# Kernel tuning notes

Hardware: AMD Instinct MI355X
Metric: run time of the kernel (lower is better)

Reference implementation:

```python
import jax, jax.numpy as jnp
import numpy as np

DIM = 128; D_STATE = 16; D_CONV = 4; EXPAND = 2
D_INNER = DIM * EXPAND            # 256
DT_RANK = (DIM + 15) // 16        # 8
B, H, W = 2, 56, 56


def _ln(x, w, b):
    m = jnp.mean(x, -1, keepdims=True)
    v = jnp.var(x, -1, keepdims=True)
    return (x - m) * jax.lax.rsqrt(v + 1e-5) * w + b


def _mamba(x, in_w, conv_w, conv_b, xproj_w, dt_w, dt_b, A_log, Dp, out_w):
    # x: (B, L, DIM)
    Bb, L, _ = x.shape
    xz = x @ in_w.T                                   # (B,L,2*D_INNER)
    xi, z = jnp.split(xz, 2, axis=-1)
    # causal depthwise conv1d (pad left d_conv-1, truncate to L)
    xc = jnp.transpose(xi, (0, 2, 1))                 # (B,D_INNER,L)
    xc = jax.lax.conv_general_dilated(
        xc, conv_w, (1,), [(D_CONV - 1, 0)],
        dimension_numbers=('NCH', 'OIH', 'NCH'),
        feature_group_count=D_INNER) + conv_b[None, :, None]
    xs = jax.nn.silu(jnp.transpose(xc, (0, 2, 1)))    # (B,L,D_INNER)
    dbl = xs @ xproj_w.T                              # (B,L,DT_RANK+2*D_STATE)
    dt = jax.nn.softplus(dbl[..., :DT_RANK] @ dt_w.T + dt_b)   # (B,L,D_INNER)
    Bc = dbl[..., DT_RANK:DT_RANK + D_STATE]          # (B,L,D_STATE)
    Cc = dbl[..., DT_RANK + D_STATE:]                 # (B,L,D_STATE)
    A = -jnp.exp(A_log)                               # (D_INNER,D_STATE)
    dA = jnp.exp(dt[..., None] * A)                   # (B,L,D_INNER,D_STATE)
    dBu = (dt * xs)[..., None] * Bc[:, :, None, :]    # (B,L,D_INNER,D_STATE)

    def step(h, inp):
        a, bu, c = inp
        h = a * h + bu                                # (B,D_INNER,D_STATE)
        return h, jnp.einsum('bdn,bn->bd', h, c)

    h0 = jnp.zeros((Bb, D_INNER, D_STATE), x.dtype)
    _, ys = jax.lax.scan(step, h0, (jnp.moveaxis(dA, 1, 0),
                                    jnp.moveaxis(dBu, 1, 0),
                                    jnp.moveaxis(Cc, 1, 0)))
    y = jnp.moveaxis(ys, 0, 1) + xs * Dp              # (B,L,D_INNER)
    y = y * jax.nn.silu(z)
    return y @ out_w.T                                # (B,L,DIM)


def _forward(x, norm_h_w, norm_h_b, norm_v_w, norm_v_b,
             dw_w, dw_b, pw_w, pw_b,
             h_in_w, h_conv_w, h_conv_b, h_xproj_w, h_dt_w, h_dt_b, h_A_log, h_D, h_out_w,
             v_in_w, v_conv_w, v_conv_b, v_xproj_w, v_dt_w, v_dt_b, v_A_log, v_D, v_out_w,
             ca_fc1_w, ca_fc2_w):
    Bb, C, Hh, Ww = x.shape
    # local branch: depthwise 3x3 + GELU + 1x1
    lf = jax.lax.conv_general_dilated(
        x, dw_w, (1, 1), [(1, 1), (1, 1)],
        dimension_numbers=('NCHW', 'OIHW', 'NCHW'),
        feature_group_count=C) + dw_b[None, :, None, None]
    lf = jax.nn.gelu(lf, approximate=False)
    lf = jnp.einsum('bchw,oc->bohw', lf, pw_w[:, :, 0, 0]) + pw_b[None, :, None, None]
    # horizontal scan: row-major tokens
    xh = _ln(x.reshape(Bb, C, Hh * Ww).transpose(0, 2, 1), norm_h_w, norm_h_b)
    oh = _mamba(xh, h_in_w, h_conv_w, h_conv_b, h_xproj_w, h_dt_w, h_dt_b,
                h_A_log, h_D, h_out_w)
    oh = oh.transpose(0, 2, 1).reshape(Bb, C, Hh, Ww)
    # vertical scan: column-major tokens
    xv = _ln(jnp.transpose(x, (0, 1, 3, 2)).reshape(Bb, C, Ww * Hh).transpose(0, 2, 1),
             norm_v_w, norm_v_b)
    ov = _mamba(xv, v_in_w, v_conv_w, v_conv_b, v_xproj_w, v_dt_w, v_dt_b,
                v_A_log, v_D, v_out_w)
    ov = jnp.transpose(ov.transpose(0, 2, 1).reshape(Bb, C, Ww, Hh), (0, 1, 3, 2))
    fused = oh + ov + lf
    # channel attention
    y = jnp.mean(fused, axis=(2, 3))                  # (B,C)
    y = jax.nn.sigmoid(jax.nn.relu(y @ ca_fc1_w.T) @ ca_fc2_w.T)
    return fused * y[:, :, None, None] + x


def setup_inputs() -> dict:
    key = jax.random.key(0)
    ks = iter(jax.random.split(key, 64))
    def nrm(shape, scale):
        return jax.random.normal(next(ks), shape, jnp.float32) * scale
    d = {}
    d['x'] = nrm((B, DIM, H, W), 1.0)
    d['norm_h_w'] = jnp.ones((DIM,), jnp.float32); d['norm_h_b'] = jnp.zeros((DIM,), jnp.float32)
    d['norm_v_w'] = jnp.ones((DIM,), jnp.float32); d['norm_v_b'] = jnp.zeros((DIM,), jnp.float32)
    d['dw_w'] = nrm((DIM, 1, 3, 3), 1.0 / 3.0)
    d['dw_b'] = jnp.zeros((DIM,), jnp.float32)
    d['pw_w'] = nrm((DIM, DIM, 1, 1), DIM ** -0.5)
    d['pw_b'] = jnp.zeros((DIM,), jnp.float32)
    for p in ('h', 'v'):
        d[p + '_in_w'] = nrm((2 * D_INNER, DIM), DIM ** -0.5)
        d[p + '_conv_w'] = nrm((D_INNER, 1, D_CONV), D_CONV ** -0.5)
        d[p + '_conv_b'] = jnp.zeros((D_INNER,), jnp.float32)
        d[p + '_xproj_w'] = nrm((DT_RANK + 2 * D_STATE, D_INNER), D_INNER ** -0.5)
        d[p + '_dt_w'] = nrm((D_INNER, DT_RANK), DT_RANK ** -0.5)
        d[p + '_dt_b'] = jnp.full((D_INNER,), -2.0, jnp.float32)  # small positive dt
        d[p + '_A_log'] = jnp.log(jnp.tile(jnp.arange(1, D_STATE + 1, dtype=jnp.float32), (D_INNER, 1)))
        d[p + '_D'] = jnp.ones((D_INNER,), jnp.float32)
        d[p + '_out_w'] = nrm((DIM, D_INNER), D_INNER ** -0.5)
    d['ca_fc1_w'] = nrm((DIM // 4, DIM), DIM ** -0.5)
    d['ca_fc2_w'] = nrm((DIM, DIM // 4), (DIM // 4) ** -0.5)
    return d


def reference(x, norm_h_w, norm_h_b, norm_v_w, norm_v_b,
              dw_w, dw_b, pw_w, pw_b,
              h_in_w, h_conv_w, h_conv_b, h_xproj_w, h_dt_w, h_dt_b, h_A_log, h_D, h_out_w,
              v_in_w, v_conv_w, v_conv_b, v_xproj_w, v_dt_w, v_dt_b, v_A_log, v_D, v_out_w,
              ca_fc1_w, ca_fc2_w):
    return _forward(x, norm_h_w, norm_h_b, norm_v_w, norm_v_b,
                    dw_w, dw_b, pw_w, pw_b,
                    h_in_w, h_conv_w, h_conv_b, h_xproj_w, h_dt_w, h_dt_b, h_A_log, h_D, h_out_w,
                    v_in_w, v_conv_w, v_conv_b, v_xproj_w, v_dt_w, v_dt_b, v_A_log, v_D, v_out_w,
                    ca_fc1_w, ca_fc2_w)
```

## Files before the change

### kernel.cpp

```cpp
#include <hip/hip_runtime.h>
#include <hip/hip_bf16.h>

typedef __hip_bfloat16 bf16;
__device__ __forceinline__ float b2f(bf16 v){ return __bfloat162float(v); }
__device__ __forceinline__ bf16 f2b(float v){ return __float2bfloat16(v); }

typedef __attribute__((ext_vector_type(8))) short frag_ab;
typedef __attribute__((ext_vector_type(4))) float frag_cd;
typedef __attribute__((ext_vector_type(4))) short short4v;

__device__ __forceinline__ frag_ab ld_frag_2xb64(const bf16* p){
  union { frag_ab f; short4v h[2]; } u;
  u.h[0] = *reinterpret_cast<const short4v*>(p);
  u.h[1] = *reinterpret_cast<const short4v*>(p+4);
  return u.f;
}

#define LLEN 3136
#define BATCH 2
#define NCHUNK 49
#define LC 64

__global__ void k_front(const float* __restrict__ x, const float* __restrict__ dww,
                        const float* __restrict__ dwb, bf16* __restrict__ tmp,
                        const float* nhw_, const float* nhb_, const float* nvw_,
                        const float* nvb_, bf16* __restrict__ xln,
                        float* __restrict__ YMEAN){
  int blk = blockIdx.x;
  int tid = threadIdx.x;
  if (blk < 1024){
    int bc = blk & 255;
    int seg = blk >> 8;
    int c = bc & 127;
    if (bc == 0 && seg == 0 && tid < 256) YMEAN[tid] = 0.f;
    const float* xp = x + (size_t)bc*LLEN;
    float w[9];
    #pragma unroll
    for (int i=0;i<9;i++) w[i] = dww[c*9+i];
    float bias = dwb[c];
    int pstart = seg * 784;
    for (int p = pstart + tid; p < pstart + 784; p += 256){
      int i = p/56, j = p%56;
      float acc = bias;
      #pragma unroll
      for (int a=0;a<3;a++){
        int ii = i + a - 1;
        if (ii < 0 || ii >= 56) continue;
        #pragma unroll
        for (int bb=0;bb<3;bb++){
          int jj = j + bb - 1;
          if (jj < 0 || jj >= 56) continue;
          acc += w[a*3+bb] * xp[ii*56+jj];
        }
      }
      float g = 0.5f*acc*(1.0f + erff(acc*0.70710678118654752f));
      tmp[(size_t)bc*LLEN + p] = f2b(g);
    }
  } else {
    int idx2 = blk - 1024;
    int h = idx2 % 56, b = idx2 / 56;
    __shared__ float sx[128][57];
    __shared__ float smean[56], srstd[56];
    __shared__ float wh[128], bh[128], wv_[128], bv_[128];
    if (tid < 128){ wh[tid]=nhw_[tid]; bh[tid]=nhb_[tid];
                    wv_[tid]=nvw_[tid]; bv_[tid]=nvb_[tid]; }
    for (int idx = tid; idx < 128*56; idx += 256){
      int c = idx / 56, w = idx % 56;
      sx[c][w] = x[((size_t)(b*128+c))*LLEN + h*56 + w];
    }
    __syncthreads();
    if (tid < 56){
      float s=0.f, s2=0.f;
      for (int c=0;c<128;c++){ float v = sx[c][tid]; s+=v; s2+=v*v; }
      float m = s*(1.f/128.f);
      float var = s2*(1.f/128.f) - m*m;
      smean[tid]=m; srstd[tid]=rsqrtf(var+1e-5f);
    }
    __syncthreads();
    bf16* outh = xln;
    bf16* outv = xln + (size_t)BATCH*LLEN*128;
    for (int idx = tid; idx < 56*128; idx += 256){
      int w = idx >> 7, c = idx & 127;
      float v = (sx[c][w]-smean[w])*srstd[w];
      outh[((size_t)b*LLEN + h*56 + w)*128 + c] = f2b(v*wh[c]+bh[c]);
      outv[((size_t)b*LLEN + w*56 + h)*128 + c] = f2b(v*wv_[c]+bv_[c]);
    }
  }
}

__global__ void k_inproj(const bf16* __restrict__ xln, const float* __restrict__ hw,
                         const float* __restrict__ vw, bf16* __restrict__ XI, bf16* __restrict__ Z){
  int dir = blockIdx.z;
  const bf16* A = xln + (size_t)dir*BATCH*LLEN*128;
  const float* W = dir ? vw : hw;
  int m0 = blockIdx.x*64;
  int npair = blockIdx.y*128;
  __shared__ __align__(16) bf16 sA[64][136];
  __shared__ __align__(16) bf16 sW[64][136];
  int tid = threadIdx.x;
  #pragma unroll
  for (int r=0;r<4;r++){
    int idx = tid + r*256;
    int row = idx >> 4, c8 = (idx & 15)*8;
    *reinterpret_cast<float4*>(&sA[row][c8]) =
        *reinterpret_cast<const float4*>(&A[(size_t)(m0+row)*128 + c8]);
  }
  int wv2 = tid >> 6, lane = tid & 63;
  int qd = lane >> 4, mr = lane & 15;
  bf16* dst = (npair < 256) ? XI : Z;
  int nbase0 = npair & 255;
  size_t dslab = (size_t)dir*BATCH*LLEN*256;
  #pragma unroll
  for (int nt=0; nt<2; nt++){
    int n0 = npair + nt*64;
    __syncthreads();
    #pragma unroll
    for (int r=0;r<8;r++){
      int idx = tid + r*256;
      int row = idx >> 5, c4 = (idx & 31)*4;
      float4 w4 = *reinterpret_cast<const float4*>(&W[(size_t)(n0+row)*128 + c4]);
      bf16 t4[4] = {f2b(w4.x), f2b(w4.y), f2b(w4.z), f2b(w4.w)};
      *reinterpret_cast<double*>(&sW[row][c4]) = *reinterpret_cast<double*>(t4);
    }
    __syncthreads();
    frag_cd acc[4] = {};
    #pragma unroll
    for (int k0=0;k0<128;k0+=32){
      frag_ab af = *reinterpret_cast<frag_ab*>(&sA[wv2*16+mr][k0+qd*8]);
      #pragma unroll
      for (int t=0;t<4;t++){
        frag_ab bfr = *reinterpret_cast<frag_ab*>(&sW[t*16+mr][k0+qd*8]);
        acc[t] = __builtin_amdgcn_mfma_f32_16x16x32_bf16(af, bfr, acc[t], 0, 0, 0);
      }
    }
    int nb = nbase0 + nt*64;
    #pragma unroll
    for (int t=0;t<4;t++)
      #pragma unroll
      for (int r=0;r<4;r++){
        int row = m0 + wv2*16 + qd*4 + r;
        int col = nb + t*16 + mr;
        dst[dslab + (size_t)row*256 + col] = f2b(acc[t][r]);
      }
  }
}

__global__ void k_dbl(const bf16* __restrict__ XI,
                      const float* hcw, const float* hcb, const float* vcw, const float* vcb,
                      const float* __restrict__ hx, const float* __restrict__ vx,
                      const float* hdw, const float* vdw, const float* hdb, const float* vdb,
                      bf16* __restrict__ XS2, bf16* __restrict__ DT2,
                      float* __restrict__ Bf, float* __restrict__ Cf){
  int m0 = blockIdx.x*64;
  int bd = m0 / LLEN;
  int l0m = m0 % LLEN;
  int dirq = bd >> 1;
  const bf16* XId = XI + (size_t)bd*LLEN*256;
  const float* W = dirq ? vx : hx;
  const float* cw = dirq ? vcw : hcw;
  const float* cb = dirq ? vcb : hcb;
  __shared__ __align__(16) bf16 sA[67][264];
  __shared__ __align__(16) bf16 sW[48][264];
  __shared__ float sdbl[64][49];
  int tid = threadIdx.x;
  for (int idx = tid; idx < 67*32; idx += 256){
    int row = idx >> 5, c8 = (idx & 31)*8;
    int l = l0m - 3 + row;
    float4 v = make_float4(0.f,0.f,0.f,0.f);
    if (l >= 0) v = *reinterpret_cast<const float4*>(&XId[(size_t)l*256 + c8]);
    *reinterpret_cast<float4*>(&sA[row][c8]) = v;
  }
  #pragma unroll
  for (int r=0;r<12;r++){
    int idx = tid + r*256;
    int row = idx >> 6, c4 = (idx & 63)*4;
    bf16 t4[4] = {f2b(0.f), f2b(0.f), f2b(0.f), f2b(0.f)};
    if (row < 40){
      float4 w4 = *reinterpret_cast<const float4*>(&W[(size_t)row*256 + c4]);
      t4[0]=f2b(w4.x); t4[1]=f2b(w4.y); t4[2]=f2b(w4.z); t4[3]=f2b(w4.w);
    }
    *reinterpret_cast<double*>(&sW[row][c4]) = *reinterpret_cast<double*>(t4);
  }
  __syncthreads();
  {
    float w0=cw[tid*4], w1=cw[tid*4+1], w2=cw[tid*4+2], w3=cw[tid*4+3];
    float cbias = cb[tid];
    size_t x2base = ((size_t)bd*16 + (tid>>4))*LLEN + l0m;
    int c16 = tid & 15;
    float xm3 = b2f(sA[0][tid]), xm2 = b2f(sA[1][tid]), xm1 = b2f(sA[2][tid]);
    #pragma unroll 4
    for (int j=0;j<64;j++){
      float x0 = b2f(sA[j+3][tid]);
      float acc = cbias + w0*xm3 + w1*xm2 + w2*xm1 + w3*x0;
      float s = acc / (1.f + __expf(-acc));
      bf16 sv = f2b(s);
      sA[j][tid] = sv;
      XS2[(x2base + j)*16 + c16] = sv;
      xm3=xm2; xm2=xm1; xm1=x0;
    }
  }
  __syncthreads();
  int wv2 = tid >> 6, lane = tid & 63;
  int qd = lane >> 4, mr = lane & 15;
  frag_cd acc[3] = {};
  #pragma unroll
  for (int k0=0;k0<256;k0+=32){
    frag_ab af = *reinterpret_cast<frag_ab*>(&sA[wv2*16+mr][k0+qd*8]);
    #pragma unroll
    for (int t=0;t<3;t++){
      frag_ab bfr = *reinterpret_cast<frag_ab*>(&sW[t*16+mr][k0+qd*8]);
      acc[t] = __builtin_amdgcn_mfma_f32_16x16x32_bf16(af, bfr, acc[t], 0, 0, 0);
    }
  }
  #pragma unroll
  for (int t=0;t<3;t++)
    #pragma unroll
    for (int r=0;r<4;r++){
      int col = t*16 + mr;
      if (col < 40) sdbl[wv2*16 + qd*4 + r][col] = acc[t][r];
    }
  __syncthreads();
  const float* dtw = dirq ? vdw : hdw;
  const float* dtb = dirq ? vdb : hdb;
  float w8[8];
  #pragma unroll
  for (int r=0;r<8;r++) w8[r] = dtw[tid*8+r];
  float biasv = dtb[tid];
  size_t d2base = ((size_t)bd*16 + (tid>>4))*LLEN + l0m;
  int c16 = tid & 15;
  for (int row=0; row<64; row++){
    float a = biasv;
    #pragma unroll
    for (int r=0;r<8;r++) a += sdbl[row][r]*w8[r];
    float sv = (a > 20.f) ? a : __logf(1.f + __expf(a));
    DT2[(d2base + row)*16 + c16] = f2b(sv);
  }
  #pragma unroll
  for (int r=0;r<8;r++){
    int idx = tid + r*256;
    int row = idx >> 5, o = idx & 31;
    float v = sdbl[row][8+o];
    size_t rr = (size_t)(m0+row)*16;
    if (o < 16) Bf[rr + o] = v;
    else        Cf[rr + (o-16)] = v;
  }
}

__global__ void k_scan1(const bf16* __restrict__ DT2, const bf16* __restrict__ XS2,
                        const float* __restrict__ Bc, const float* hA, const float* vA,
                        float* __restrict__ Pbuf, float* __restrict__ Hbuf){
  int bd = blockIdx.z;
  int g  = blockIdx.y;
  int ck = blockIdx.x;
  int l0 = ck*LC;
  const float* Bd = Bc + (size_t)bd*LLEN*16;
  const float* Alog = (bd >> 1) ? vA : hA;
  int tid = threadIdx.x;
  int dl = tid >> 4, n = tid & 15;
  float A = -__expf(Alog[(g*16+dl)*16+n]);
  __shared__ float sdt[LC][16], sxs[LC][16], sB[LC][16];
  size_t base2 = (((size_t)bd*16 + g)*LLEN + l0)*16;
  #pragma unroll
  for (int r=0;r<4;r++){
    int idx = tid + r*256;
    sdt[idx>>4][idx&15] = b2f(DT2[base2 + idx]);
    sxs[idx>>4][idx&15] = b2f(XS2[base2 + idx]);
    (&sB[0][0])[idx] = Bd[(size_t)l0*16 + idx];
  }
  __syncthreads();
  float h = 0.f, P = 1.f;
  #pragma unroll 8
  for (int i=0;i<LC;i++){
    float a = sdt[i][dl];
    float u = sxs[i][dl];
    float dA = __expf(a * A);
    h = dA*h + (a*u)*sB[i][n];
    P *= dA;
  }
  size_t sidx = (((size_t)bd*16 + g)*NCHUNK + ck)*256 + tid;
  Pbuf[sidx] = P;
  Hbuf[sidx] = h;
}

__global__ void k_scan2(const float* __restrict__ Pbuf, float* __restrict__ Hbuf){
  int q = blockIdx.x;
  int tid = threadIdx.x;
  float carry = 0.f;
  #pragma unroll 7
  for (int k=0;k<NCHUNK;k++){
    size_t idx = ((size_t)q*NCHUNK + k)*256 + tid;
    float Pv = Pbuf[idx];
    float He = Hbuf[idx];
    Hbuf[idx] = carry;
    carry = Pv*carry + He;
  }
}

__global__ void k_scan3(const bf16* __restrict__ DT2, const bf16* __restrict__ XS2,
                        const float* __restrict__ Bc, const float* __restrict__ Cc,
                        const float* hA, const float* vA,
                        const float* __restrict__ Hbuf, bf16* __restrict__ ys){
  int bd = blockIdx.z;
  int g  = blockIdx.y;
  int ck = blockIdx.x;
  int l0 = ck*LC;
  const float* Bd = Bc + (size_t)bd*LLEN*16;
  const float* Cd = Cc + (size_t)bd*LLEN*16;
  bf16* yd = ys + (size_t)bd*LLEN*256;
  const float* Alog = (bd >> 1) ? vA : hA;
  int tid = threadIdx.x;
  int dl = tid >> 4, n = tid & 15;
  float A = -__expf(Alog[(g*16+dl)*16+n]);
  __shared__ float sdt[LC][16], sxs[LC][16], sB[LC][16], sC[LC][16];
  __shared__ float sp2[16][272];
  size_t base2 = (((size_t)bd*16 + g)*LLEN + l0)*16;
  #pragma unroll
  for (int r=0;r<4;r++){
    int idx = tid + r*256;
    sdt[idx>>4][idx&15] = b2f(DT2[base2 + idx]);
    sxs[idx>>4][idx&15] = b2f(XS2[base2 + idx]);
    (&sB[0][0])[idx] = Bd[(size_t)l0*16 + idx];
    (&sC[0][0])[idx] = Cd[(size_t)l0*16 + idx];
  }
  size_t sidx = (((size_t)bd*16 + g)*NCHUNK + ck)*256 + tid;
  float h = Hbuf[sidx];
  __syncthreads();
  int swz = dl*17 + n;
  int i_local = tid >> 4;
  int c16 = tid & 15;
  int rbase = c16*17;
  for (int i0=0; i0<LC; i0+=16){
    #pragma unroll
    for (int ii=0;ii<16;ii++){
      int i = i0 + ii;
      float a = sdt[i][dl];
      float u = sxs[i][dl];
      float dA = __expf(a * A);
      h = dA*h + (a*u)*sB[i][n];
      sp2[ii][swz] = h * sC[i][n];
    }
    __syncthreads();
    const float* row = &sp2[i_local][rbase];
    float s = 0.f;
    #pragma unroll
    for (int k=0;k<16;k++) s += row[k];
    yd[(size_t)(l0+i0+i_local)*256 + g*16 + c16] = f2b(s);
    __syncthreads();
  }
}

__global__ void k_outgemm(const bf16* __restrict__ ys, const bf16* __restrict__ XS2,
                          const bf16* __restrict__ Z, const float* __restrict__ hD,
                          const float* __restrict__ vD, const float* __restrict__ how,
                          const float* __restrict__ vow, bf16* __restrict__ OD){
  int dir = blockIdx.y;
  size_t slab = (size_t)dir*BATCH*LLEN*256;
  const float* W = dir ? vow : how;
  const float* Dw = dir ? vD : hD;
  bf16* od = OD + (size_t)dir*BATCH*LLEN*128;
  int m0 = blockIdx.x*32;
  int bd = dir*2 + m0/LLEN;
  int lbase = m0 % LLEN;
  __shared__ __align__(16) bf16 sA[32][264];
  __shared__ __align__(16) bf16 sW[64][264];
  int tid = threadIdx.x;
  #pragma unroll
  for (int r=0;r<4;r++){
    int idx = tid + r*256;
    int row = idx >> 5, c8 = (idx & 31)*8;
    size_t e = slab + (size_t)(m0+row)*256 + c8;
    size_t e2 = (((size_t)bd*16 + (c8>>4))*LLEN + lbase + row)*16 + (c8&15);
    bf16 yb[8], xb[8], zb[8], ob[8];
    *reinterpret_cast<float4*>(yb) = *reinterpret_cast<const float4*>(&ys[e]);
    *reinterpret_cast<float4*>(xb) = *reinterpret_cast<const float4*>(&XS2[e2]);
    *reinterpret_cast<float4*>(zb) = *reinterpret_cast<const float4*>(&Z[e]);
    #pragma unroll
    for (int j=0;j<8;j++){
      float Dv = Dw[c8 + j];
      float yv = b2f(yb[j]) + b2f(xb[j])*Dv;
      float zv = b2f(zb[j]);
      ob[j] = f2b(yv * (zv/(1.f+__expf(-zv))));
    }
    *reinterpret_cast<float4*>(&sA[row][c8]) = *reinterpret_cast<float4*>(ob);
  }
  int wv2 = tid >> 6, lane = tid & 63;
  int qd = lane >> 4, mr = lane & 15;
  int msub = wv2 & 1, tpair = (wv2 >> 1)*2;
  #pragma unroll
  for (int nh=0; nh<2; nh++){
    int n0 = nh*64;
    __syncthreads();
    #pragma unroll
    for (int r=0;r<16;r++){
      int idx = tid + r*256;
      int row = idx >> 6, c4 = (idx & 63)*4;
      float4 w4 = *reinterpret_cast<const float4*>(&W[(size_t)(n0+row)*256 + c4]);
      bf16 t4[4] = {f2b(w4.x), f2b(w4.y), f2b(w4.z), f2b(w4.w)};
      *reinterpret_cast<double*>(&sW[row][c4]) = *reinterpret_cast<double*>(t4);
    }
    __syncthreads();
    frag_cd acc[2] = {};
    #pragma unroll
    for (int k0=0;k0<256;k0+=32){
      frag_ab af = *reinterpret_cast<frag_ab*>(&sA[msub*16+mr][k0+qd*8]);
      #pragma unroll
      for (int i=0;i<2;i++){
        frag_ab bfr = *reinterpret_cast<frag_ab*>(&sW[(tpair+i)*16+mr][k0+qd*8]);
        acc[i] = __builtin_amdgcn_mfma_f32_16x16x32_bf16(af, bfr, acc[i], 0, 0, 0);
      }
    }
    #pragma unroll
    for (int i=0;i<2;i++)
      #pragma unroll
      for (int r=0;r<4;r++){
        int row = m0 + msub*16 + qd*4 + r;
        int col = n0 + (tpair+i)*16 + mr;
        od[(size_t)row*128 + col] = f2b(acc[i][r]);
      }
  }
}

__global__ void k_pwcomb(const bf16* __restrict__ tmp, const float* __restrict__ pww,
                         const float* __restrict__ pwb, const bf16* __restrict__ OD,
                         float* __restrict__ fused, float* __restrict__ YMEAN){
  int p0 = blockIdx.x * 64;
  int m0 = blockIdx.y * 64;
  int b  = blockIdx.z;
  const bf16* T = tmp + (size_t)b*128*LLEN;
  const bf16* od0 = OD + (size_t)b*LLEN*128;
  const bf16* od1 = OD + (size_t)(BATCH + b)*LLEN*128;
  __shared__ __align__(16) bf16 sA[64][136];
  __shared__ __align__(16) bf16 sBt[64][132];
  __shared__ float sOD[64][65];
  int tid = threadIdx.x;
  #pragma unroll
  for (int r=0;r<8;r++){
    int idx = tid + r*256;
    int row = idx >> 5, c4 = (idx & 31)*4;
    float4 w4 = *reinterpret_cast<const float4*>(&pww[(size_t)(m0+row)*128 + c4]);
    bf16 t4[4] = {f2b(w4.x), f2b(w4.y), f2b(w4.z), f2b(w4.w)};
    *reinterpret_cast<double*>(&sA[row][c4]) = *reinterpret_cast<double*>(t4);
  }
  #pragma unroll
  for (int r=0;r<8;r++){
    int idx = tid + r*256;
    int c = idx >> 4, p4 = (idx & 15)*4;
    union { double d; bf16 v[4]; } u;
    u.d = *reinterpret_cast<const double*>(&T[(size_t)c*LLEN + p0 + p4]);
    #pragma unroll
    for (int j=0;j<4;j++) sBt[p4+j][c] = u.v[j];
  }
  #pragma unroll
  for (int r=0;r<8;r++){
    int idx = tid + r*256;
    int prow = idx >> 5, mp = (idx & 31)*2;
    int p = p0 + prow;
    int pi = p/56, pj = p%56;
    int pt = pj*56 + pi;
    bf16 a0[2], a1[2];
    *reinterpret_cast<float*>(a0) = *reinterpret_cast<const float*>(&od0[(size_t)p*128 + m0 + mp]);
    *reinterpret_cast<float*>(a1) = *reinterpret_cast<const float*>(&od1[(size_t)pt*128 + m0 + mp]);
    sOD[prow][mp]   = b2f(a0[0]) + b2f(a1[0]);
    sOD[prow][mp+1] = b2f(a0[1]) + b2f(a1[1]);
  }
  __syncthreads();
  int wv2 = tid >> 6, lane = tid & 63;
  int qd = lane >> 4, mr = lane & 15;
  frag_cd acc[4] = {};
  #pragma unroll
  for (int k0=0;k0<128;k0+=32){
    frag_ab af = *reinterpret_cast<frag_ab*>(&sA[wv2*16+mr][k0+qd*8]);
    #pragma unroll
    for (int t=0;t<4;t++){
      frag_ab bfr = ld_frag_2xb64(&sBt[t*16+mr][k0+qd*8]);
      acc[t] = __builtin_amdgcn_mfma_f32_16x16x32_bf16(af, bfr, acc[t], 0, 0, 0);
    }
  }
  #pragma unroll
  for (int r=0;r<4;r++){
    int m = m0 + wv2*16 + qd*4 + r;
    float bias = pwb[m];
    float s = 0.f;
    #pragma unroll
    for (int t=0;t<4;t++){
      int p = p0 + t*16 + mr;
      float val = acc[t][r] + bias + sOD[t*16+mr][m - m0];
      fused[((size_t)b*128 + m)*LLEN + p] = val;
      s += val;
    }
    s += __shfl_xor(s, 1, 16);
    s += __shfl_xor(s, 2, 16);
    s += __shfl_xor(s, 4, 16);
    s += __shfl_xor(s, 8, 16);
    if (mr == 0) atomicAdd(&YMEAN[b*128 + m], s);
  }
}

__global__ void k_final_gate(const float* __restrict__ fused, const float* __restrict__ YMEAN,
                             const float* __restrict__ fc1, const float* __restrict__ fc2,
                             const float* __restrict__ x, float* __restrict__ out){
  int bc = blockIdx.x;
  int b = bc >> 7, c = bc & 127;
  __shared__ float ym[128], s1[32];
  __shared__ float gsh;
  int tid = threadIdx.x;
  if (tid < 128) ym[tid] = YMEAN[b*128 + tid] * (1.f/(float)LLEN);
  __syncthreads();
  {
    int o = tid >> 3, part = tid & 7;
    float a = 0.f;
    #pragma unroll
    for (int k=0;k<16;k++) a += ym[part*16 + k] * fc1[o*128 + part*16 + k];
    a += __shfl_xor(a, 1, 8);
    a += __shfl_xor(a, 2, 8);
    a += __shfl_xor(a, 4, 8);
    if (part == 0) s1[o] = fmaxf(a, 0.f);
  }
  __syncthreads();
  if (tid < 32){
    float a = s1[tid] * fc2[c*32 + tid];
    a += __shfl_xor(a, 1, 32);
    a += __shfl_xor(a, 2, 32);
    a += __shfl_xor(a, 4, 32);
    a += __shfl_xor(a, 8, 32);
    a += __shfl_xor(a, 16, 32);
    if (tid == 0) gsh = 1.f/(1.f+__expf(-a));
  }
  __syncthreads();
  float g = gsh;
  const float4* f4 = reinterpret_cast<const float4*>(fused) + (size_t)bc*784;
  const float4* x4 = reinterpret_cast<const float4*>(x) + (size_t)bc*784;
  float4* o4 = reinterpret_cast<float4*>(out) + (size_t)bc*784;
  #pragma unroll
  for (int it=0; it<4; it++){
    int p = it*256 + tid;
    if (p < 784){
      float4 fv = f4[p], xv = x4[p];
      o4[p] = make_float4(fv.x*g+xv.x, fv.y*g+xv.y, fv.z*g+xv.z, fv.w*g+xv.w);
    }
  }
}

extern "C" void kernel_launch(void* const* d_in, const int* in_sizes, int n_in,
                              void* d_out, int out_size, void* d_ws, size_t ws_size,
                              hipStream_t stream) {
  const float* x      = (const float*)d_in[0];
  const float* nhw    = (const float*)d_in[1];
  const float* nhb    = (const float*)d_in[2];
  const float* nvw    = (const float*)d_in[3];
  const float* nvb    = (const float*)d_in[4];
  const float* dww    = (const float*)d_in[5];
  const float* dwb    = (const float*)d_in[6];
  const float* pww    = (const float*)d_in[7];
  const float* pwb    = (const float*)d_in[8];
  const float* h_inw  = (const float*)d_in[9];
  const float* h_cw   = (const float*)d_in[10];
  const float* h_cb   = (const float*)d_in[11];
  const float* h_xw   = (const float*)d_in[12];
  const float* h_dtw  = (const float*)d_in[13];
  const float* h_dtb  = (const float*)d_in[14];
  const float* h_Al   = (const float*)d_in[15];
  const float* h_D    = (const float*)d_in[16];
  const float* h_ow   = (const float*)d_in[17];
  const float* v_inw  = (const float*)d_in[18];
  const float* v_cw   = (const float*)d_in[19];
  const float* v_cb   = (const float*)d_in[20];
  const float* v_xw   = (const float*)d_in[21];
  const float* v_dtw  = (const float*)d_in[22];
  const float* v_dtb  = (const float*)d_in[23];
  const float* v_Al   = (const float*)d_in[24];
  const float* v_D    = (const float*)d_in[25];
  const float* v_ow   = (const float*)d_in[26];
  const float* fc1    = (const float*)d_in[27];
  const float* fc2    = (const float*)d_in[28];

  float* FUSED = (float*)d_out;
  float* out   = (float*)d_out;

  char* base = (char*)d_ws;
  bf16*  XLN   = (bf16*)(base + 1605632);
  bf16*  DT2   = (bf16*)(base + 0);
  bf16*  OD    = (bf16*)(base + 0);
  bf16*  XI    = (bf16*)(base + 6422528);
  bf16*  YS    = (bf16*)(base + 6422528);
  bf16*  Z     = (bf16*)(base + 12845056);
  bf16*  XS2   = (bf16*)(base + 19267584);
  float* Bf    = (float*)(base + 25690112);
  float* Cf    = (float*)(base + 26492928);
  float* Hbuf  = (float*)(base + 27295744);
  float* YMEAN = (float*)(base + 30507008);
  bf16*  TMP   = (bf16*)(base + 30508032);
  float* Pbuf  = (float*)(base + 32113664);

  k_front<<<dim3(1024 + 56*BATCH), dim3(256), 0, stream>>>(x, dww, dwb, TMP,
                                                           nhw, nhb, nvw, nvb, XLN, YMEAN);
  k_inproj<<<dim3(98,4,2), dim3(256), 0, stream>>>(XLN, h_inw, v_inw, XI, Z);
  k_dbl<<<dim3(196), dim3(256), 0, stream>>>(XI, h_cw, h_cb, v_cw, v_cb,
                                             h_xw, v_xw, h_dtw, v_dtw, h_dtb, v_dtb,
                                             XS2, DT2, Bf, Cf);
  k_scan1<<<dim3(NCHUNK,16,4), dim3(256), 0, stream>>>(DT2, XS2, Bf, h_Al, v_Al, Pbuf, Hbuf);
  k_scan2<<<dim3(64), dim3(256), 0, stream>>>(Pbuf, Hbuf);
  k_scan3<<<dim3(NCHUNK,16,4), dim3(256), 0, stream>>>(DT2, XS2, Bf, Cf, h_Al, v_Al, Hbuf, YS);
  k_outgemm<<<dim3(196,2), dim3(256), 0, stream>>>(YS, XS2, Z, h_D, v_D, h_ow, v_ow, OD);
  k_pwcomb<<<dim3(49,2,BATCH), dim3(256), 0, stream>>>(TMP, pww, pwb, OD, FUSED, YMEAN);
  k_final_gate<<<dim3(256), dim3(256), 0, stream>>>(FUSED, YMEAN, fc1, fc2, x, out);
}
```

Before: 221.9 us.

## Fuse scan carry pass into scan1 and channel gate into pwcomb via atomics

The separate carry-propagation kernel is removed: the last chunk block per (batch,group) queue, detected with an atomic counter, runs the sequential carry pass inside k_scan1. The final gate kernel is also fused into k_pwcomb. The last block per batch computes the squeeze-excite gate and publishes it through a flag, the other blocks spin-wait on it and then write the gated residual output directly from registers. This removes two launches and the round trip of the fused tensor through global memory. In exchange it relies on all 196 pwcomb blocks being co-resident to avoid deadlock and serialises the carry pass onto one block per queue.

```diff
diff --git a/kernel.cpp b/kernel.cpp
--- a/kernel.cpp
+++ b/kernel.cpp
@@ -25,14 +25,17 @@
                         const float* __restrict__ dwb, bf16* __restrict__ tmp,
                         const float* nhw_, const float* nhb_, const float* nvw_,
                         const float* nvb_, bf16* __restrict__ xln,
-                        float* __restrict__ YMEAN){
+                        float* __restrict__ YMEAN, int* __restrict__ ZCNT){
   int blk = blockIdx.x;
   int tid = threadIdx.x;
   if (blk < 1024){
     int bc = blk & 255;
     int seg = blk >> 8;
     int c = bc & 127;
-    if (bc == 0 && seg == 0 && tid < 256) YMEAN[tid] = 0.f;
+    if (blk == 0){
+      if (tid < 256) YMEAN[tid] = 0.f;
+      if (tid < 68)  ZCNT[tid] = 0;
+    }
     const float* xp = x + (size_t)bc*LLEN;
     float w[9];
     #pragma unroll
@@ -248,7 +251,8 @@
 
 __global__ void k_scan1(const bf16* __restrict__ DT2, const bf16* __restrict__ XS2,
                         const float* __restrict__ Bc, const float* hA, const float* vA,
-                        float* __restrict__ Pbuf, float* __restrict__ Hbuf){
+                        float* __restrict__ Pbuf, float* __restrict__ Hbuf,
+                        int* __restrict__ CNT){
   int bd = blockIdx.z;
   int g  = blockIdx.y;
   int ck = blockIdx.x;
@@ -277,22 +281,25 @@
     h = dA*h + (a*u)*sB[i][n];
     P *= dA;
   }
-  size_t sidx = (((size_t)bd*16 + g)*NCHUNK + ck)*256 + tid;
+  int q = bd*16 + g;
+  size_t sidx = ((size_t)q*NCHUNK + ck)*256 + tid;
   Pbuf[sidx] = P;
   Hbuf[sidx] = h;
-}
-
-__global__ void k_scan2(const float* __restrict__ Pbuf, float* __restrict__ Hbuf){
-  int q = blockIdx.x;
-  int tid = threadIdx.x;
-  float carry = 0.f;
-  #pragma unroll 7
-  for (int k=0;k<NCHUNK;k++){
-    size_t idx = ((size_t)q*NCHUNK + k)*256 + tid;
-    float Pv = Pbuf[idx];
-    float He = Hbuf[idx];
-    Hbuf[idx] = carry;
-    carry = Pv*carry + He;
+  __threadfence();
+  __shared__ int slast;
+  if (tid == 0) slast = (atomicAdd(&CNT[q], 1) == NCHUNK-1);
+  __syncthreads();
+  if (slast){
+    __threadfence();
+    float carry = 0.f;
+    #pragma unroll 7
+    for (int k=0;k<NCHUNK;k++){
+      size_t idx = ((size_t)q*NCHUNK + k)*256 + tid;
+      float Pv = Pbuf[idx];
+      float He = Hbuf[idx];
+      Hbuf[idx] = carry;
+      carry = Pv*carry + He;
+    }
   }
 }
 
@@ -422,7 +429,10 @@
 
 __global__ void k_pwcomb(const bf16* __restrict__ tmp, const float* __restrict__ pww,
                          const float* __restrict__ pwb, const bf16* __restrict__ OD,
-                         float* __restrict__ fused, float* __restrict__ YMEAN){
+                         const float* __restrict__ x, float* __restrict__ out,
+                         float* __restrict__ YMEAN, int* __restrict__ CNTPW,
+                         int* __restrict__ FLAG, float* __restrict__ GATE,
+                         const float* __restrict__ fc1, const float* __restrict__ fc2){
   int p0 = blockIdx.x * 64;
   int m0 = blockIdx.y * 64;
   int b  = blockIdx.z;
@@ -432,6 +442,8 @@
   __shared__ __align__(16) bf16 sA[64][136];
   __shared__ __align__(16) bf16 sBt[64][132];
   __shared__ float sOD[64][65];
+  __shared__ float ym[128], s1g[32];
+  __shared__ int slast;
   int tid = threadIdx.x;
   #pragma unroll
   for (int r=0;r<8;r++){
@@ -476,6 +488,7 @@
       acc[t] = __builtin_amdgcn_mfma_f32_16x16x32_bf16(af, bfr, acc[t], 0, 0, 0);
     }
   }
+  float vals[4][4];
   #pragma unroll
   for (int r=0;r<4;r++){
     int m = m0 + wv2*16 + qd*4 + r;
@@ -483,9 +496,8 @@
     float s = 0.f;
     #pragma unroll
     for (int t=0;t<4;t++){
-      int p = p0 + t*16 + mr;
       float val = acc[t][r] + bias + sOD[t*16+mr][m - m0];
-      fused[((size_t)b*128 + m)*LLEN + p] = val;
+      vals[t][r] = val;
       s += val;
     }
     s += __shfl_xor(s, 1, 16);
@@ -494,51 +506,58 @@
     s += __shfl_xor(s, 8, 16);
     if (mr == 0) atomicAdd(&YMEAN[b*128 + m], s);
   }
-}
-
-__global__ void k_final_gate(const float* __restrict__ fused, const float* __restrict__ YMEAN,
-                             const float* __restrict__ fc1, const float* __restrict__ fc2,
-                             const float* __restrict__ x, float* __restrict__ out){
-  int bc = blockIdx.x;
-  int b = bc >> 7, c = bc & 127;
-  __shared__ float ym[128], s1[32];
-  __shared__ float gsh;
-  int tid = threadIdx.x;
-  if (tid < 128) ym[tid] = YMEAN[b*128 + tid] * (1.f/(float)LLEN);
-  __syncthreads();
-  {
-    int o = tid >> 3, part = tid & 7;
-    float a = 0.f;
-    #pragma unroll
-    for (int k=0;k<16;k++) a += ym[part*16 + k] * fc1[o*128 + part*16 + k];
-    a += __shfl_xor(a, 1, 8);
-    a += __shfl_xor(a, 2, 8);
-    a += __shfl_xor(a, 4, 8);
-    if (part == 0) s1[o] = fmaxf(a, 0.f);
-  }
-  __syncthreads();
-  if (tid < 32){
-    float a = s1[tid] * fc2[c*32 + tid];
-    a += __shfl_xor(a, 1, 32);
-    a += __shfl_xor(a, 2, 32);
-    a += __shfl_xor(a, 4, 32);
-    a += __shfl_xor(a, 8, 32);
-    a += __shfl_xor(a, 16, 32);
-    if (tid == 0) gsh = 1.f/(1.f+__expf(-a));
-  }
-  __syncthreads();
-  float g = gsh;
-  const float4* f4 = reinterpret_cast<const float4*>(fused) + (size_t)bc*784;
-  const float4* x4 = reinterpret_cast<const float4*>(x) + (size_t)bc*784;
-  float4* o4 = reinterpret_cast<float4*>(out) + (size_t)bc*784;
-  #pragma unroll
-  for (int it=0; it<4; it++){
-    int p = it*256 + tid;
-    if (p < 784){
-      float4 fv = f4[p], xv = x4[p];
-      o4[p] = make_float4(fv.x*g+xv.x, fv.y*g+xv.y, fv.z*g+xv.z, fv.w*g+xv.w);
-    }
-  }
+  __threadfence();
+  if (tid == 0) slast = (atomicAdd(&CNTPW[b], 1) == 2*49 - 1);
+  __syncthreads();
+  if (slast){
+    __threadfence();
+    if (tid < 128)
+      ym[tid] = __hip_atomic_load(&YMEAN[b*128+tid], __ATOMIC_RELAXED,
+                                  __HIP_MEMORY_SCOPE_AGENT) * (1.f/(float)LLEN);
+    __syncthreads();
+    {
+      int o = tid >> 3, part = tid & 7;
+      float a = 0.f;
+      #pragma unroll
+      for (int k=0;k<16;k++) a += ym[part*16 + k] * fc1[o*128 + part*16 + k];
+      a += __shfl_xor(a, 1, 8);
+      a += __shfl_xor(a, 2, 8);
+      a += __shfl_xor(a, 4, 8);
+      if (part == 0) s1g[o] = fmaxf(a, 0.f);
+    }
+    __syncthreads();
+    if (tid < 128){
+      float a = 0.f;
+      #pragma unroll
+      for (int j=0;j<32;j++) a += s1g[j]*fc2[tid*32+j];
+      __hip_atomic_store(&GATE[b*128+tid], 1.f/(1.f+__expf(-a)),
+                         __ATOMIC_RELAXED, __HIP_MEMORY_SCOPE_AGENT);
+    }
+    __threadfence();
+    __syncthreads();
+    if (tid == 0)
+      __hip_atomic_store(&FLAG[b], 1, __ATOMIC_RELEASE, __HIP_MEMORY_SCOPE_AGENT);
+  } else {
+    if (tid == 0)
+      while (__hip_atomic_load(&FLAG[b], __ATOMIC_ACQUIRE, __HIP_MEMORY_SCOPE_AGENT) == 0)
+        __builtin_amdgcn_s_sleep(2);
+  }
+  __syncthreads();
+  float g4[4];
+  #pragma unroll
+  for (int r=0;r<4;r++){
+    int m = m0 + wv2*16 + qd*4 + r;
+    g4[r] = __hip_atomic_load(&GATE[b*128+m], __ATOMIC_RELAXED, __HIP_MEMORY_SCOPE_AGENT);
+  }
+  #pragma unroll
+  for (int t=0;t<4;t++)
+    #pragma unroll
+    for (int r=0;r<4;r++){
+      int m = m0 + wv2*16 + qd*4 + r;
+      int p = p0 + t*16 + mr;
+      size_t i = ((size_t)b*128 + m)*LLEN + p;
+      out[i] = vals[t][r]*g4[r] + x[i];
+    }
 }
 
 extern "C" void kernel_launch(void* const* d_in, const int* in_sizes, int n_in,
@@ -574,8 +593,7 @@
   const float* fc1    = (const float*)d_in[27];
   const float* fc2    = (const float*)d_in[28];
 
-  float* FUSED = (float*)d_out;
-  float* out   = (float*)d_out;
+  float* out = (float*)d_out;
 
   char* base = (char*)d_ws;
   bf16*  XLN   = (bf16*)(base + 1605632);
@@ -591,17 +609,21 @@
   float* YMEAN = (float*)(base + 30507008);
   bf16*  TMP   = (bf16*)(base + 30508032);
   float* Pbuf  = (float*)(base + 32113664);
+  int*   ZCNT  = (int*)  (base + 35324928);
+  float* GATE  = (float*)(base + 35325440);
+  int*   CNTS  = ZCNT;
+  int*   CNTPW = ZCNT + 64;
+  int*   FLAG  = ZCNT + 66;
 
   k_front<<<dim3(1024 + 56*BATCH), dim3(256), 0, stream>>>(x, dww, dwb, TMP,
-                                                           nhw, nhb, nvw, nvb, XLN, YMEAN);
+                                                           nhw, nhb, nvw, nvb, XLN, YMEAN, ZCNT);
   k_inproj<<<dim3(98,4,2), dim3(256), 0, stream>>>(XLN, h_inw, v_inw, XI, Z);
   k_dbl<<<dim3(196), dim3(256), 0, stream>>>(XI, h_cw, h_cb, v_cw, v_cb,
                                              h_xw, v_xw, h_dtw, v_dtw, h_dtb, v_dtb,
                                              XS2, DT2, Bf, Cf);
-  k_scan1<<<dim3(NCHUNK,16,4), dim3(256), 0, stream>>>(DT2, XS2, Bf, h_Al, v_Al, Pbuf, Hbuf);
-  k_scan2<<<dim3(64), dim3(256), 0, stream>>>(Pbuf, Hbuf);
+  k_scan1<<<dim3(NCHUNK,16,4), dim3(256), 0, stream>>>(DT2, XS2, Bf, h_Al, v_Al, Pbuf, Hbuf, CNTS);
   k_scan3<<<dim3(NCHUNK,16,4), dim3(256), 0, stream>>>(DT2, XS2, Bf, Cf, h_Al, v_Al, Hbuf, YS);
   k_outgemm<<<dim3(196,2), dim3(256), 0, stream>>>(YS, XS2, Z, h_D, v_D, h_ow, v_ow, OD);
-  k_pwcomb<<<dim3(49,2,BATCH), dim3(256), 0, stream>>>(TMP, pww, pwb, OD, FUSED, YMEAN);
-  k_final_gate<<<dim3(256), dim3(256), 0, stream>>>(FUSED, YMEAN, fc1, fc2, x, out);
-}
+  k_pwcomb<<<dim3(49,2,BATCH), dim3(256), 0, stream>>>(TMP, pww, pwb, OD, x, out,
+                                                       YMEAN, CNTPW, FLAG, GATE, fc1, fc2);
+}
```

New measurement: 514.1 us. 132% more time.
